# Performance work log

Hardware: AMD Instinct MI355X
Metric: run time of the kernel (lower is better)

The kernel has to match this reference:

```python
import jax, jax.numpy as jnp
import numpy as np

VAR_N, LEVELS, NCELLS, PRED_N = 4, 17, 56, 12
D = VAR_N * LEVELS          # 68
FLAT = VAR_N * D            # 272 = ntiles * interm in CrossConnector
T = 4096
DT = 0.1                    # fused-ODE solver step of the LTC cell


def _var_encoder(x, w1, b1, w2, b2, w3, b3, w4, b4, w5, b5):
    # nn.Sequential(Linear, ReLU, Linear, ReLU, Linear, ReLU, Linear, ReLU, Linear)
    h = jax.nn.relu(x @ w1 + b1)
    h = jax.nn.relu(h @ w2 + b2)
    h = jax.nn.relu(h @ w3 + b3)
    h = jax.nn.relu(h @ w4 + b4)
    return h @ w5 + b5


def _run_ltc(seq, wx, wh, b, a, tau, wout, bout):
    def cell(h, u):
        f = jax.nn.sigmoid(u @ wx + h @ wh + b)           # gated synaptic activation
        return (h + DT * f * a) / (1.0 + DT * (1.0 / (tau + 0.5) + f))

    def step_obs(h, u):
        h2 = cell(h, u)
        return h2, h2 @ wout + bout

    hT, vs1 = jax.lax.scan(step_obs, jnp.zeros((NCELLS,), seq.dtype), seq)

    def step_pred(carry, _):
        h, v = carry
        h2 = cell(h, v)
        v2 = h2 @ wout + bout
        return (h2, v2), v2

    _, vs2 = jax.lax.scan(step_pred, (hT, vs1[-1]), None, length=PRED_N)
    return jnp.concatenate([vs1, vs2], axis=0)        # (T+PRED_N, LEVELS)


def setup_inputs() -> dict:
    key = jax.random.key(0)
    ks = iter(jax.random.split(key, 64))
    d = {"x": jax.random.normal(next(ks), (T, D), jnp.float32)}

    def add_ve(prefix, inp, out):
        dims = [(inp, inp), (inp, inp), (inp, out), (out, out), (out, out)]
        for i, (fi, fo) in enumerate(dims, 1):
            d[f"{prefix}w{i}"] = jax.random.normal(next(ks), (fi, fo), jnp.float32) / np.sqrt(fi)
            d[f"{prefix}b{i}"] = jax.random.normal(next(ks), (fo,), jnp.float32) * 0.01

    add_ve("p", D, D)          # preproc  VarEncoder(68,68)
    add_ve("c1", LEVELS, D)    # CrossConnector inner VarEncoder(17,68)
    add_ve("c2", FLAT, D)      # CrossConnector outer VarEncoder(272,68)

    d["ltc_wx"] = jax.random.normal(next(ks), (VAR_N, LEVELS, NCELLS), jnp.float32) / np.sqrt(LEVELS)
    d["ltc_wh"] = jax.random.normal(next(ks), (VAR_N, NCELLS, NCELLS), jnp.float32) / np.sqrt(NCELLS)
    d["ltc_b"] = jax.random.normal(next(ks), (VAR_N, NCELLS), jnp.float32) * 0.01
    d["ltc_a"] = jax.random.normal(next(ks), (VAR_N, NCELLS), jnp.float32)
    d["ltc_tau"] = jax.random.uniform(next(ks), (VAR_N, NCELLS), jnp.float32)
    d["ltc_wout"] = jax.random.normal(next(ks), (VAR_N, NCELLS, LEVELS), jnp.float32) / np.sqrt(NCELLS)
    d["ltc_bout"] = jax.random.normal(next(ks), (VAR_N, LEVELS), jnp.float32) * 0.01
    return d


def reference(x, pw1, pb1, pw2, pb2, pw3, pb3, pw4, pb4, pw5, pb5,
              c1w1, c1b1, c1w2, c1b2, c1w3, c1b3, c1w4, c1b4, c1w5, c1b5,
              c2w1, c2b1, c2w2, c2b2, c2w3, c2b3, c2w4, c2b4, c2w5, c2b5,
              ltc_wx, ltc_wh, ltc_b, ltc_a, ltc_tau, ltc_wout, ltc_bout):
    pre = _var_encoder(x, pw1, pb1, pw2, pb2, pw3, pb3, pw4, pb4, pw5, pb5)   # (T, 68)
    xs = pre.reshape(VAR_N, -1, LEVELS)                                       # (4, T, 17) row-major, as torch.reshape
    vs = jax.vmap(_run_ltc)(xs, ltc_wx, ltc_wh, ltc_b, ltc_a, ltc_tau,
                            ltc_wout, ltc_bout)                               # (4, T+12, 17)
    vs = jnp.transpose(vs, (1, 0, 2))                                         # (T+12, 4, 17)
    y = jax.nn.relu(_var_encoder(vs, c1w1, c1b1, c1w2, c1b2, c1w3, c1b3,
                                 c1w4, c1b4, c1w5, c1b5))                     # (T+12, 4, 68)
    y = y.reshape(y.shape[0], -1)                                             # (T+12, 272)
    return _var_encoder(y, c2w1, c2b1, c2w2, c2b2, c2w3, c2b3,
                        c2w4, c2b4, c2w5, c2b5)                               # (T+12, 68)
```

## Files before the change

kernel.cpp:

```cpp
#include <hip/hip_runtime.h>
#include <hip/hip_bf16.h>
#include <math.h>

#define VAR_N 4
#define LEVELS 17
#define NCELLS 56
#define PRED_N 12
#define TSTEPS 4096
#define DT 0.1f
#define RPB 8
#define LOG2E 1.44269504088896340736f

static __device__ __forceinline__ float rl(float x, int lane) {
    return __int_as_float(__builtin_amdgcn_readlane(__float_as_int(x), lane));
}
static __device__ __forceinline__ float rcpf(float x) {
    return __builtin_amdgcn_rcpf(x);
}

template <int S>
__global__ void mlp5_kernel(const float* __restrict__ in, float* __restrict__ out,
                            const float* __restrict__ w1, const float* __restrict__ b1,
                            const float* __restrict__ w2, const float* __restrict__ b2,
                            const float* __restrict__ w3, const float* __restrict__ b3,
                            const float* __restrict__ w4, const float* __restrict__ b4,
                            const float* __restrict__ w5, const float* __restrict__ b5,
                            int nrows, int d0, int d1, int d2, int d3, int d4, int d5,
                            int relu_last) {
    extern __shared__ float lds[];
    float* bufA = lds;
    float* bufB = lds + RPB * S;
    const int r0 = blockIdx.x * RPB;
    const int tid = threadIdx.x;
    const int bt = blockDim.x;

    for (int idx = tid; idx < RPB * d0; idx += bt) {
        int r = idx / d0, c = idx - r * d0;
        int gr = r0 + r;
        bufA[r * S + c] = (gr < nrows) ? in[(size_t)gr * d0 + c] : 0.f;
    }
    __syncthreads();

    const float* Ws[5] = {w1, w2, w3, w4, w5};
    const float* Bs[5] = {b1, b2, b3, b4, b5};
    int dins[5] = {d0, d1, d2, d3, d4};
    int douts[5] = {d1, d2, d3, d4, d5};

    for (int L = 0; L < 5; ++L) {
        const float* __restrict__ W = Ws[L];
        const float* __restrict__ B = Bs[L];
        const int din = dins[L], dout = douts[L];
        const bool act = (L < 4) || (relu_last != 0);
        for (int j = tid; j < dout; j += bt) {
            float acc[RPB];
            float bj = B[j];
#pragma unroll
            for (int r = 0; r < RPB; ++r) acc[r] = bj;
            for (int k = 0; k < din; ++k) {
                float wv = W[(size_t)k * dout + j];
#pragma unroll
                for (int r = 0; r < RPB; ++r)
                    acc[r] = fmaf(bufA[r * S + k], wv, acc[r]);
            }
#pragma unroll
            for (int r = 0; r < RPB; ++r) {
                float vo = acc[r];
                if (act) vo = fmaxf(vo, 0.f);
                bufB[r * S + j] = vo;
            }
        }
        __syncthreads();
        float* t = bufA; bufA = bufB; bufB = t;
    }

    for (int idx = tid; idx < RPB * d5; idx += bt) {
        int r = idx / d5, c = idx - r * d5;
        int gr = r0 + r;
        if (gr < nrows) out[(size_t)gr * d5 + c] = bufA[r * S + c];
    }
}

__global__ void gprep_kernel(const float* __restrict__ pre, const float* __restrict__ wx,
                             const float* __restrict__ b, float* __restrict__ g) {
    int idx = blockIdx.x * blockDim.x + threadIdx.x;
    if (idx >= VAR_N * NCELLS * TSTEPS) return;
    int t = idx % TSTEPS;
    int rem = idx / TSTEPS;
    int j = rem % NCELLS;
    int v = rem / NCELLS;
    const float* u = pre + (size_t)(v * 1024 + (t >> 2)) * 68 + (t & 3) * LEVELS;
    float acc = b[v * NCELLS + j];
#pragma unroll
    for (int l = 0; l < LEVELS; ++l)
        acc = fmaf(u[l], wx[(v * LEVELS + l) * NCELLS + j], acc);
    g[idx] = acc * LOG2E;
}

__global__ void __launch_bounds__(64, 1) scan_kernel(
    const float* __restrict__ g, const float* __restrict__ wh,
    const float* __restrict__ a, const float* __restrict__ tau,
    const float* __restrict__ wx, const float* __restrict__ wout,
    const float* __restrict__ bout, const float* __restrict__ b,
    float* __restrict__ H, float* __restrict__ vs_t) {
    typedef float v2 __attribute__((ext_vector_type(2)));
    const int v = blockIdx.x;
    const int lane = threadIdx.x;
    const bool active = lane < NCELLS;
    const int j = active ? lane : (NCELLS - 1);
    __shared__ __align__(16) float hbuf[64];

    v2 whp[28];
#pragma unroll
    for (int q = 0; q < 28; ++q) {
        float w0 = active ? wh[((size_t)v * NCELLS + 2 * q + 0) * NCELLS + lane] * LOG2E : 0.f;
        float w1 = active ? wh[((size_t)v * NCELLS + 2 * q + 1) * NCELLS + lane] * LOG2E : 0.f;
        v2 t; t.x = w0; t.y = w1;
        whp[q] = t;
    }
    const float alpha = active ? DT * a[v * NCELLS + lane] : 0.f;
    const float cden = active ? 1.f + DT / (tau[v * NCELLS + lane] + 0.5f) : 1.f;

    const float4* __restrict__ gv4 = (const float4*)(g + ((size_t)v * NCELLS + j) * TSTEPS);
    float* __restrict__ hp = H + (size_t)v * TSTEPS * NCELLS + lane;

    auto cell = [&](float h, float gcur) -> float {
        hbuf[lane] = h;
        const float4* h4 = (const float4*)hbuf;
        float4 hv[14];
#pragma unroll
        for (int q = 0; q < 14; ++q) hv[q] = h4[q];
        v2 a0 = {0.f, 0.f}, a1 = {0.f, 0.f}, a2 = {0.f, 0.f}, a3 = {0.f, 0.f};
#pragma unroll
        for (int q = 0; q < 7; ++q) {
            float4 hq0 = hv[2 * q];
            float4 hq1 = hv[2 * q + 1];
            v2 p0; p0.x = hq0.x; p0.y = hq0.y;
            v2 p1; p1.x = hq0.z; p1.y = hq0.w;
            v2 p2; p2.x = hq1.x; p2.y = hq1.y;
            v2 p3; p3.x = hq1.z; p3.y = hq1.w;
            a0 = __builtin_elementwise_fma(p0, whp[4 * q + 0], a0);
            a1 = __builtin_elementwise_fma(p1, whp[4 * q + 1], a1);
            a2 = __builtin_elementwise_fma(p2, whp[4 * q + 2], a2);
            a3 = __builtin_elementwise_fma(p3, whp[4 * q + 3], a3);
        }
        v2 s = (a0 + a1) + (a2 + a3);
        float z2 = gcur + s.x + s.y;
        float e = __builtin_amdgcn_exp2f(-z2);
        float f = rcpf(1.f + e);
        return fmaf(alpha, f, h) * rcpf(fmaf(DT, f, cden));
    };

    float h = 0.f;
    float4 gq = gv4[0];
    for (int tq = 0; tq < TSTEPS / 4; ++tq) {
        float4 gn = gq;
        if (tq + 1 < TSTEPS / 4) gn = gv4[tq + 1];
        h = cell(h, gq.x); if (active) hp[0 * NCELLS] = h;
        h = cell(h, gq.y); if (active) hp[1 * NCELLS] = h;
        h = cell(h, gq.z); if (active) hp[2 * NCELLS] = h;
        h = cell(h, gq.w); if (active) hp[3 * NCELLS] = h;
        hp += 4 * NCELLS;
        gq = gn;
    }

    float wxcol[LEVELS];
#pragma unroll
    for (int l = 0; l < LEVELS; ++l)
        wxcol[l] = active ? wx[(v * LEVELS + l) * NCELLS + lane] * LOG2E : 0.f;
    float wtc[NCELLS];
#pragma unroll
    for (int jj = 0; jj < NCELLS; ++jj)
        wtc[jj] = (lane < LEVELS) ? wout[((size_t)v * NCELLS + jj) * LEVELS + lane] : 0.f;
    const float bj = active ? b[v * NCELLS + lane] * LOG2E : 0.f;
    const float boutl = (lane < LEVELS) ? bout[v * LEVELS + lane] : 0.f;

    float vv = boutl;
#pragma unroll
    for (int jj = 0; jj < NCELLS; ++jj) vv = fmaf(rl(h, jj), wtc[jj], vv);

    for (int i = 0; i < PRED_N; ++i) {
        float z2 = bj;
#pragma unroll
        for (int l = 0; l < LEVELS; ++l) z2 = fmaf(rl(vv, l), wxcol[l], z2);
#pragma unroll
        for (int k = 0; k < NCELLS; ++k) {
            float wk = (k & 1) ? whp[k >> 1].y : whp[k >> 1].x;
            z2 = fmaf(rl(h, k), wk, z2);
        }
        float e = __builtin_amdgcn_exp2f(-z2);
        float f = rcpf(1.f + e);
        h = fmaf(alpha, f, h) * rcpf(fmaf(DT, f, cden));
        vv = boutl;
#pragma unroll
        for (int jj = 0; jj < NCELLS; ++jj) vv = fmaf(rl(h, jj), wtc[jj], vv);
        if (lane < LEVELS)
            vs_t[((size_t)(TSTEPS + i) * VAR_N + v) * LEVELS + lane] = vv;
    }
}

__global__ void proj_kernel(const float* __restrict__ H, const float* __restrict__ wout,
                            const float* __restrict__ bout, float* __restrict__ vs_t) {
    int idx = blockIdx.x * blockDim.x + threadIdx.x;
    if (idx >= VAR_N * TSTEPS * LEVELS) return;
    int l = idx % LEVELS;
    int rem = idx / LEVELS;
    int t = rem % TSTEPS;
    int v = rem / TSTEPS;
    const float* hrow = H + ((size_t)v * TSTEPS + t) * NCELLS;
    float acc = bout[v * LEVELS + l];
#pragma unroll
    for (int jj = 0; jj < NCELLS; ++jj)
        acc = fmaf(hrow[jj], wout[(v * NCELLS + jj) * LEVELS + l], acc);
    vs_t[((size_t)t * VAR_N + v) * LEVELS + l] = acc;
}

extern "C" void kernel_launch(void* const* d_in, const int* in_sizes, int n_in,
                              void* d_out, int out_size, void* d_ws, size_t ws_size,
                              hipStream_t stream) {
    const float* x = (const float*)d_in[0];
    const float* pw[5] = {(const float*)d_in[1], (const float*)d_in[3], (const float*)d_in[5],
                          (const float*)d_in[7], (const float*)d_in[9]};
    const float* pb[5] = {(const float*)d_in[2], (const float*)d_in[4], (const float*)d_in[6],
                          (const float*)d_in[8], (const float*)d_in[10]};
    const float* c1w[5] = {(const float*)d_in[11], (const float*)d_in[13], (const float*)d_in[15],
                           (const float*)d_in[17], (const float*)d_in[19]};
    const float* c1b[5] = {(const float*)d_in[12], (const float*)d_in[14], (const float*)d_in[16],
                           (const float*)d_in[18], (const float*)d_in[20]};
    const float* c2w[5] = {(const float*)d_in[21], (const float*)d_in[23], (const float*)d_in[25],
                           (const float*)d_in[27], (const float*)d_in[29]};
    const float* c2b[5] = {(const float*)d_in[22], (const float*)d_in[24], (const float*)d_in[26],
                           (const float*)d_in[28], (const float*)d_in[30]};
    const float* ltc_wx = (const float*)d_in[31];
    const float* ltc_wh = (const float*)d_in[32];
    const float* ltc_b = (const float*)d_in[33];
    const float* ltc_a = (const float*)d_in[34];
    const float* ltc_tau = (const float*)d_in[35];
    const float* ltc_wout = (const float*)d_in[36];
    const float* ltc_bout = (const float*)d_in[37];

    float* ws = (float*)d_ws;
    float* pre = ws;
    float* g = pre + 278528;
    float* H = g + 917504;
    float* vs_t = H + 917504;
    float* y1 = vs_t + 279344;
    float* out = (float*)d_out;

    const int TROWS = TSTEPS + PRED_N;

    {
        int nrows = TSTEPS;
        int blocks = (nrows + RPB - 1) / RPB;
        size_t shmem = 2 * RPB * 68 * sizeof(float);
        mlp5_kernel<68><<<blocks, 256, shmem, stream>>>(
            x, pre, pw[0], pb[0], pw[1], pb[1], pw[2], pb[2], pw[3], pb[3], pw[4], pb[4],
            nrows, 68, 68, 68, 68, 68, 68, 0);
    }
    {
        int n = VAR_N * NCELLS * TSTEPS;
        gprep_kernel<<<(n + 255) / 256, 256, 0, stream>>>(pre, ltc_wx, ltc_b, g);
    }
    scan_kernel<<<VAR_N, 64, 0, stream>>>(g, ltc_wh, ltc_a, ltc_tau, ltc_wx,
                                          ltc_wout, ltc_bout, ltc_b, H, vs_t);
    {
        int n = VAR_N * TSTEPS * LEVELS;
        proj_kernel<<<(n + 255) / 256, 256, 0, stream>>>(H, ltc_wout, ltc_bout, vs_t);
    }
    {
        int nrows = TROWS * VAR_N;
        int blocks = (nrows + RPB - 1) / RPB;
        size_t shmem = 2 * RPB * 68 * sizeof(float);
        mlp5_kernel<68><<<blocks, 256, shmem, stream>>>(
            vs_t, y1, c1w[0], c1b[0], c1w[1], c1b[1], c1w[2], c1b[2], c1w[3], c1b[3],
            c1w[4], c1b[4], nrows, 17, 17, 17, 68, 68, 68, 1);
    }
    {
        int nrows = TROWS;
        int blocks = (nrows + RPB - 1) / RPB;
        size_t shmem = 2 * RPB * 272 * sizeof(float);
        mlp5_kernel<272><<<blocks, 256, shmem, stream>>>(
            y1, out, c2w[0], c2b[0], c2w[1], c2b[1], c2w[2], c2b[2], c2w[3], c2b[3],
            c2w[4], c2b[4], nrows, 272, 272, 272, 68, 68, 68, 0);
    }
}
```

Measured before the change: 1.213 ms.

## Parallelize MLP over rows and outputs, simplify LTC cell algebra

The MLP kernel now processes 16 rows per block and gives each thread one (row, output) pair, reading activations as float4, instead of looping over 8 rows per output column. The LTC cell update is rewritten algebraically: multiplying numerator and denominator by (1+e) drops one reciprocal from the serial recurrence. The exponent input is clamped at -80 to avoid overflow. Scheduling barriers are added to interleave the DS reads, VMEM and VALU work inside the recurrence. Per-thread weight reuse across rows is lost, and the scheduling hints may conflict with the compiler's own ordering.

```diff
diff --git a/kernel.cpp b/kernel.cpp
--- a/kernel.cpp
+++ b/kernel.cpp
@@ -8,7 +8,7 @@
 #define PRED_N 12
 #define TSTEPS 4096
 #define DT 0.1f
-#define RPB 8
+#define RPB 16
 #define LOG2E 1.44269504088896340736f
 
 static __device__ __forceinline__ float rl(float x, int lane) {
@@ -51,23 +51,22 @@
         const float* __restrict__ B = Bs[L];
         const int din = dins[L], dout = douts[L];
         const bool act = (L < 4) || (relu_last != 0);
-        for (int j = tid; j < dout; j += bt) {
-            float acc[RPB];
-            float bj = B[j];
-#pragma unroll
-            for (int r = 0; r < RPB; ++r) acc[r] = bj;
-            for (int k = 0; k < din; ++k) {
-                float wv = W[(size_t)k * dout + j];
-#pragma unroll
-                for (int r = 0; r < RPB; ++r)
-                    acc[r] = fmaf(bufA[r * S + k], wv, acc[r]);
+        for (int idx = tid; idx < RPB * dout; idx += bt) {
+            int r = idx / dout, j = idx - r * dout;
+            float acc = B[j];
+            const float* __restrict__ arow = bufA + r * S;
+            int k = 0;
+            for (; k + 4 <= din; k += 4) {
+                const float4 hx = *(const float4*)(arow + k);
+                acc = fmaf(hx.x, W[(size_t)(k + 0) * dout + j],
+                       fmaf(hx.y, W[(size_t)(k + 1) * dout + j],
+                        fmaf(hx.z, W[(size_t)(k + 2) * dout + j],
+                         fmaf(hx.w, W[(size_t)(k + 3) * dout + j], acc))));
             }
-#pragma unroll
-            for (int r = 0; r < RPB; ++r) {
-                float vo = acc[r];
-                if (act) vo = fmaxf(vo, 0.f);
-                bufB[r * S + j] = vo;
-            }
+            for (; k < din; ++k)
+                acc = fmaf(arow[k], W[(size_t)k * dout + j], acc);
+            if (act) acc = fmaxf(acc, 0.f);
+            bufB[r * S + j] = acc;
         }
         __syncthreads();
         float* t = bufA; bufA = bufB; bufB = t;
@@ -144,10 +143,17 @@
             a3 = __builtin_elementwise_fma(p3, whp[4 * q + 3], a3);
         }
         v2 s = (a0 + a1) + (a2 + a3);
-        float z2 = gcur + s.x + s.y;
-        float e = __builtin_amdgcn_exp2f(-z2);
-        float f = rcpf(1.f + e);
-        return fmaf(alpha, f, h) * rcpf(fmaf(DT, f, cden));
+        float z2 = (gcur + s.x) + s.y;
+        float zc = fmaxf(z2, -80.f);
+        float e = __builtin_amdgcn_exp2f(-zc);
+        float t1 = 1.f + e;
+        float num = fmaf(h, t1, alpha);
+        float den = fmaf(cden, t1, DT);
+        float hn = num * rcpf(den);
+        __builtin_amdgcn_sched_group_barrier(0x200, 1, 0);
+        __builtin_amdgcn_sched_group_barrier(0x100, 14, 0);
+        __builtin_amdgcn_sched_group_barrier(0x002, 40, 0);
+        return hn;
     };
 
     float h = 0.f;
@@ -187,9 +193,10 @@
             float wk = (k & 1) ? whp[k >> 1].y : whp[k >> 1].x;
             z2 = fmaf(rl(h, k), wk, z2);
         }
-        float e = __builtin_amdgcn_exp2f(-z2);
-        float f = rcpf(1.f + e);
-        h = fmaf(alpha, f, h) * rcpf(fmaf(DT, f, cden));
+        float zc = fmaxf(z2, -80.f);
+        float e = __builtin_amdgcn_exp2f(-zc);
+        float t1 = 1.f + e;
+        h = fmaf(h, t1, alpha) * rcpf(fmaf(cden, t1, DT));
         vv = boutl;
 #pragma unroll
         for (int jj = 0; jj < NCELLS; ++jj) vv = fmaf(rl(h, jj), wtc[jj], vv);
```

Result: slower. 1.419 ms (+16.9%).
